# Optimization experiments

Hardware: AMD Instinct MI355X
Metric: run time of the kernel (lower is better)

Reference implementation:

```python
import jax, jax.numpy as jnp
import numpy as np

B, S, M_DIM, N_DIM, K_NNZ = 8, 2048, 2048, 2048, 205


def setup_inputs() -> dict:
    key = jax.random.key(0)
    k1, k2, k3, k4 = jax.random.split(key, 4)
    x = jax.random.normal(k1, (B, S, M_DIM), dtype=jnp.float32)
    # CSR structure: K_NNZ unique, sorted column indices per row
    scores = jax.random.uniform(k2, (N_DIM, M_DIM))
    cols = jnp.sort(jnp.argsort(scores, axis=1)[:, :K_NNZ], axis=1)  # [N, K] unique per row
    indices = cols.reshape(-1).astype(jnp.int32)                      # [nnz]
    indptr = (jnp.arange(N_DIM + 1) * K_NNZ).astype(jnp.int32)        # [N+1]
    W_val = jax.random.normal(k3, (N_DIM * K_NNZ,), dtype=jnp.float32) * (1.0 / np.sqrt(M_DIM))
    bias = jax.random.normal(k4, (N_DIM,), dtype=jnp.float32) * 0.01
    return {"x": x, "W_val": W_val, "bias": bias, "indices": indices, "indptr": indptr}


def reference(x, W_val, bias, indices, indptr):
    # SparseLinear.forward: y = x @ W^T + bias, with W stored in CSR
    # (W_val: nnz values, indptr: [N+1] row pointers, indices: [nnz] column ids).
    N = indptr.shape[0] - 1
    M = x.shape[-1]
    nnz = W_val.shape[0]
    # row id of each nonzero, derived from indptr (standard CSR expansion)
    row_ids = jnp.searchsorted(indptr, jnp.arange(nnz, dtype=indptr.dtype), side="right") - 1
    # materialize the sparse weight (CSR columns are unique per row -> set is exact)
    W = jnp.zeros((N, M), dtype=W_val.dtype).at[row_ids, indices].set(W_val)
    return jnp.einsum("bsm,nm->bsn", x, W) + bias
```

## Files before the change

### kernel.cpp

```cpp
#include <hip/hip_runtime.h>
#include <hip/hip_bf16.h>
#include <stdint.h>

#define M_TOT 16384
#define K_TOT 2048
#define N_TOT 2048

#define BM 128
#define BN 128
#define BK 64

#define W_BLOCKS 2048
#define CAST_BLOCKS 16384

typedef __attribute__((ext_vector_type(8))) short short8;
typedef __attribute__((ext_vector_type(4))) float float4v;
typedef __attribute__((ext_vector_type(8))) unsigned short ushort8;

__device__ __forceinline__ unsigned short f2bf_rne(float f) {
    union { float f; unsigned u; } a; a.f = f;
    unsigned r = a.u + 0x7FFFu + ((a.u >> 16) & 1u);
    return (unsigned short)(r >> 16);
}

__global__ void prep_kernel(const float* __restrict__ x,
                            const float* __restrict__ val, const int* __restrict__ idx,
                            const int* __restrict__ indptr,
                            unsigned short* __restrict__ xb, unsigned short* __restrict__ Wb) {
    const int b = blockIdx.x;
    if (b < W_BLOCKS) {
        const int n = b;
        unsigned short* row = Wb + (size_t)n * K_TOT;
        ushort8 z = {0, 0, 0, 0, 0, 0, 0, 0};
        ((ushort8*)row)[threadIdx.x] = z;
        __syncthreads();
        const int s = indptr[n], e = indptr[n + 1];
        for (int j = s + (int)threadIdx.x; j < e; j += (int)blockDim.x)
            row[idx[j]] = f2bf_rne(val[j]);
    } else {
        const int i = (b - W_BLOCKS) * 256 + (int)threadIdx.x;
        const float4* xf = (const float4*)x;
        float4 a = xf[2 * i];
        float4 c = xf[2 * i + 1];
        ushort8 o;
        o[0] = f2bf_rne(a.x); o[1] = f2bf_rne(a.y); o[2] = f2bf_rne(a.z); o[3] = f2bf_rne(a.w);
        o[4] = f2bf_rne(c.x); o[5] = f2bf_rne(c.y); o[6] = f2bf_rne(c.z); o[7] = f2bf_rne(c.w);
        ((ushort8*)xb)[i] = o;
    }
}

__global__ __launch_bounds__(256) void gemm_bias_kernel(
    const unsigned short* __restrict__ A,
    const unsigned short* __restrict__ Bw,
    const float* __restrict__ bias,
    float* __restrict__ C)
{
    __shared__ unsigned short Asm[BM * BK];
    __shared__ unsigned short Bsm[BN * BK];

    const int tid  = threadIdx.x;
    const int lane = tid & 63;
    const int wave = tid >> 6;
    const int bm = blockIdx.y;
    const int bn = blockIdx.x;

    const int srow_l = lane >> 3;
    const int schunk = ((lane & 7) ^ srow_l) * 8;
    const unsigned short* a_g[4];
    const unsigned short* b_g[4];
    unsigned short* a_l[4];
    unsigned short* b_l[4];
#pragma unroll
    for (int l = 0; l < 4; ++l) {
        const int row = wave * 32 + l * 8 + srow_l;
        a_g[l] = A  + (size_t)(bm * BM + row) * K_TOT + schunk;
        b_g[l] = Bw + (size_t)(bn * BN + row) * K_TOT + schunk;
        a_l[l] = Asm + (wave * 32 + l * 8) * BK;
        b_l[l] = Bsm + (wave * 32 + l * 8) * BK;
    }

    const int wm = (wave >> 1) * 64;
    const int wn = (wave & 1) * 64;
    const int mrow = lane & 15;
    const int quad = lane >> 4;
    const int rx   = mrow & 7;

    float4v acc[4][4] = {};

    for (int k0 = 0; k0 < K_TOT; k0 += BK) {
        __syncthreads();
#pragma unroll
        for (int l = 0; l < 4; ++l)
            __builtin_amdgcn_global_load_lds(
                (const __attribute__((address_space(1))) unsigned int*)(a_g[l] + k0),
                (__attribute__((address_space(3))) unsigned int*)a_l[l], 16, 0, 0);
#pragma unroll
        for (int l = 0; l < 4; ++l)
            __builtin_amdgcn_global_load_lds(
                (const __attribute__((address_space(1))) unsigned int*)(b_g[l] + k0),
                (__attribute__((address_space(3))) unsigned int*)b_l[l], 16, 0, 0);
        __syncthreads();

#pragma unroll
        for (int ks = 0; ks < 2; ++ks) {
            short8 af[4], bf_[4];
#pragma unroll
            for (int mi = 0; mi < 4; ++mi) {
                const int r = wm + mi * 16 + mrow;
                const int slot = (ks * 4 + quad) ^ rx;
                af[mi] = *(const short8*)(Asm + r * BK + slot * 8);
            }
#pragma unroll
            for (int ni = 0; ni < 4; ++ni) {
                const int r = wn + ni * 16 + mrow;
                const int slot = (ks * 4 + quad) ^ rx;
                bf_[ni] = *(const short8*)(Bsm + r * BK + slot * 8);
            }
#pragma unroll
            for (int mi = 0; mi < 4; ++mi)
#pragma unroll
                for (int ni = 0; ni < 4; ++ni)
                    acc[mi][ni] = __builtin_amdgcn_mfma_f32_16x16x32_bf16(
                        af[mi], bf_[ni], acc[mi][ni], 0, 0, 0);
        }
    }

#pragma unroll
    for (int ni = 0; ni < 4; ++ni) {
        const int col = bn * BN + wn + ni * 16 + mrow;
        const float bv = bias[col];
#pragma unroll
        for (int mi = 0; mi < 4; ++mi) {
#pragma unroll
            for (int r = 0; r < 4; ++r) {
                const int row = bm * BM + wm + mi * 16 + quad * 4 + r;
                C[(size_t)row * N_TOT + col] = acc[mi][ni][r] + bv;
            }
        }
    }
}

extern "C" void kernel_launch(void* const* d_in, const int* in_sizes, int n_in,
                              void* d_out, int out_size, void* d_ws, size_t ws_size,
                              hipStream_t stream) {
    const float* x       = (const float*)d_in[0];
    const float* W_val   = (const float*)d_in[1];
    const float* bias    = (const float*)d_in[2];
    const int*   indices = (const int*)d_in[3];
    const int*   indptr  = (const int*)d_in[4];
    float* out = (float*)d_out;

    unsigned short* xb = (unsigned short*)d_ws;
    unsigned short* Wb = xb + (size_t)M_TOT * K_TOT;
    if (ws_size < ((size_t)M_TOT * K_TOT + (size_t)N_TOT * K_TOT) * sizeof(unsigned short))
        return;

    prep_kernel<<<W_BLOCKS + CAST_BLOCKS, 256, 0, stream>>>(x, W_val, indices, indptr, xb, Wb);
    dim3 grid(N_TOT / BN, M_TOT / BM);
    gemm_bias_kernel<<<grid, 256, 0, stream>>>(xb, Wb, bias, out);
}
```

Measured before the change: 372.8 us.

## Add 256x256 double-buffered 8-wave GEMM with phased prefetch and tile swizzle

Adds a new GEMM kernel with 256x256 tiles, 512 threads and 128KB of dynamic LDS. It double-buffers A and B halves and interleaves global-to-LDS prefetch with MFMA phases, using barriers and explicit vmcnt waits. Block indices are remapped for L2 locality, and setprio is raised during MFMA. The aim is to hide load latency and raise arithmetic intensity, at the cost of occupancy and complex hand synchronisation. The old 128x128 kernel is kept as a fallback if the shared-memory attribute call fails.

```diff
diff --git a/kernel.cpp b/kernel.cpp
--- a/kernel.cpp
+++ b/kernel.cpp
@@ -6,9 +6,10 @@
 #define K_TOT 2048
 #define N_TOT 2048
 
-#define BM 128
-#define BN 128
+#define BM 256
+#define BN 256
 #define BK 64
+#define LDS_HALF (128 * 64)
 
 #define W_BLOCKS 2048
 #define CAST_BLOCKS 16384
@@ -49,14 +50,163 @@
     }
 }
 
-__global__ __launch_bounds__(256) void gemm_bias_kernel(
+__global__ __launch_bounds__(512, 2) void gemm_bias_kernel_256(
     const unsigned short* __restrict__ A,
     const unsigned short* __restrict__ Bw,
     const float* __restrict__ bias,
     float* __restrict__ C)
 {
-    __shared__ unsigned short Asm[BM * BK];
-    __shared__ unsigned short Bsm[BN * BK];
+    extern __shared__ unsigned short lds[];
+
+    const int tid  = threadIdx.x;
+    const int lane = tid & 63;
+    const int wave = tid >> 6;
+
+    const int raw = blockIdx.x;
+    const int lid = (raw & 7) * 64 + (raw >> 3);
+    const int bm = lid >> 3;
+    const int bn = lid & 7;
+
+    const int wrow = wave >> 2;
+    const int wcol = wave & 3;
+    const int wr16 = wrow * 16;
+    const int wc16 = wcol * 16;
+    const int mrow = lane & 15;
+    const int quad = lane >> 4;
+    const int rx   = mrow & 7;
+
+    const int srow = lane >> 3;
+    const int csrc = ((lane & 7) ^ srow) * 8;
+    const unsigned short* pA = A  + (size_t)(bm * BM + wave * 8 + srow) * K_TOT + csrc;
+    const unsigned short* pB = Bw + (size_t)(bn * BN + wave * 8 + srow) * K_TOT + csrc;
+    unsigned short* lw = lds + wave * 8 * 64;
+
+    float4v acc[8][4] = {};
+
+#define STAGE(PG, MATIDX, BUF, H, K0)                                            \
+    { _Pragma("unroll")                                                          \
+      for (int l = 0; l < 2; ++l) {                                              \
+        const unsigned short* g = (PG) + ((size_t)((H) * 128 + l * 64) * K_TOT + (size_t)(K0)); \
+        unsigned short* lp = lw + (((BUF) * 4 + (MATIDX) * 2 + (H)) * LDS_HALF) + l * 64 * 64;  \
+        __builtin_amdgcn_global_load_lds(                                        \
+            (const __attribute__((address_space(1))) unsigned int*)g,            \
+            (__attribute__((address_space(3))) unsigned int*)lp, 16, 0, 0);      \
+      } }
+
+#define WAITV4 asm volatile("s_waitcnt vmcnt(4)" ::: "memory")
+#define WAITV0 asm volatile("s_waitcnt vmcnt(0)" ::: "memory")
+#define NOSTG  ((void)0)
+#define NOWT   ((void)0)
+
+#define PHASE(BUF, MH, NH, STG, TAILW)                                           \
+  {                                                                              \
+    const unsigned short* Ah = lds + ((BUF) * 4 + (MH)) * LDS_HALF;              \
+    const unsigned short* Bh = lds + ((BUF) * 4 + 2 + (NH)) * LDS_HALF;          \
+    short8 af[4][2], bfr[2][2];                                                  \
+    _Pragma("unroll")                                                            \
+    for (int mi = 0; mi < 4; ++mi) {                                             \
+      const int r = mi * 32 + wr16 + mrow;                                       \
+      _Pragma("unroll")                                                          \
+      for (int ks = 0; ks < 2; ++ks)                                             \
+        af[mi][ks] = *(const short8*)(Ah + r * 64 + (((ks * 4 + quad) ^ rx) * 8)); \
+    }                                                                            \
+    _Pragma("unroll")                                                            \
+    for (int ni = 0; ni < 2; ++ni) {                                             \
+      const int r = ni * 64 + wc16 + mrow;                                       \
+      _Pragma("unroll")                                                          \
+      for (int ks = 0; ks < 2; ++ks)                                             \
+        bfr[ni][ks] = *(const short8*)(Bh + r * 64 + (((ks * 4 + quad) ^ rx) * 8)); \
+    }                                                                            \
+    STG;                                                                         \
+    asm volatile("" ::: "memory");                                               \
+    __builtin_amdgcn_s_barrier();                                                \
+    asm volatile("s_waitcnt lgkmcnt(0)" ::: "memory");                           \
+    __builtin_amdgcn_s_setprio(1);                                               \
+    _Pragma("unroll")                                                            \
+    for (int mi = 0; mi < 4; ++mi)                                               \
+      _Pragma("unroll")                                                          \
+      for (int ni = 0; ni < 2; ++ni)                                             \
+        _Pragma("unroll")                                                        \
+        for (int ks = 0; ks < 2; ++ks)                                           \
+          acc[(MH) * 4 + mi][(NH) * 2 + ni] =                                    \
+              __builtin_amdgcn_mfma_f32_16x16x32_bf16(                           \
+                  af[mi][ks], bfr[ni][ks], acc[(MH) * 4 + mi][(NH) * 2 + ni], 0, 0, 0); \
+    __builtin_amdgcn_s_setprio(0);                                               \
+    TAILW;                                                                       \
+    asm volatile("" ::: "memory");                                               \
+    __builtin_amdgcn_s_barrier();                                                \
+    asm volatile("" ::: "memory");                                               \
+  }
+
+    STAGE(pA, 0, 0, 0, 0);
+    STAGE(pB, 1, 0, 1, 0);
+    STAGE(pB, 1, 0, 0, 0);
+    STAGE(pA, 0, 0, 1, 0);
+    STAGE(pA, 0, 1, 0, 64);
+    STAGE(pB, 1, 1, 1, 64);
+    WAITV4;
+    asm volatile("" ::: "memory");
+    __builtin_amdgcn_s_barrier();
+    asm volatile("" ::: "memory");
+
+    int k0b = 64, k0c = 128, k0d = 192;
+#pragma unroll 1
+    for (int it = 0; it < 15; ++it) {
+        PHASE(0, 0, 0, STAGE(pB, 1, 1, 0, k0b), NOWT)
+        PHASE(0, 0, 1, STAGE(pA, 0, 1, 1, k0b), NOWT)
+        PHASE(0, 1, 1, STAGE(pA, 0, 0, 0, k0c), NOWT)
+        PHASE(0, 1, 0, STAGE(pB, 1, 0, 1, k0c), WAITV4)
+        PHASE(1, 0, 0, STAGE(pB, 1, 0, 0, k0c), NOWT)
+        PHASE(1, 0, 1, STAGE(pA, 0, 0, 1, k0c), NOWT)
+        PHASE(1, 1, 1, STAGE(pA, 0, 1, 0, k0d), NOWT)
+        PHASE(1, 1, 0, STAGE(pB, 1, 1, 1, k0d), WAITV4)
+        k0b += 128; k0c += 128; k0d += 128;
+    }
+    PHASE(0, 0, 0, STAGE(pB, 1, 1, 0, k0b), NOWT)
+    PHASE(0, 0, 1, STAGE(pA, 0, 1, 1, k0b), NOWT)
+    PHASE(0, 1, 1, NOSTG, NOWT)
+    PHASE(0, 1, 0, NOSTG, WAITV0)
+    PHASE(1, 0, 0, NOSTG, NOWT)
+    PHASE(1, 0, 1, NOSTG, NOWT)
+    PHASE(1, 1, 1, NOSTG, NOWT)
+    PHASE(1, 1, 0, NOSTG, NOWT)
+
+#pragma unroll
+    for (int nh = 0; nh < 2; ++nh)
+#pragma unroll
+        for (int ni = 0; ni < 2; ++ni) {
+            const int col = bn * BN + nh * 128 + ni * 64 + wc16 + mrow;
+            const float bv = bias[col];
+#pragma unroll
+            for (int mh = 0; mh < 2; ++mh)
+#pragma unroll
+                for (int mi = 0; mi < 4; ++mi) {
+                    const int row0 = bm * BM + mh * 128 + mi * 32 + wr16 + quad * 4;
+#pragma unroll
+                    for (int r = 0; r < 4; ++r)
+                        C[(size_t)(row0 + r) * N_TOT + col] =
+                            acc[mh * 4 + mi][nh * 2 + ni][r] + bv;
+                }
+        }
+#undef PHASE
+#undef STAGE
+#undef WAITV4
+#undef WAITV0
+#undef NOSTG
+#undef NOWT
+}
+
+#define FBM 128
+#define FBN 128
+#define FBK 64
+__global__ __launch_bounds__(256) void gemm_bias_kernel_128(
+    const unsigned short* __restrict__ A,
+    const unsigned short* __restrict__ Bw,
+    const float* __restrict__ bias,
+    float* __restrict__ C)
+{
+    __shared__ unsigned short Asm[FBM * FBK];
+    __shared__ unsigned short Bsm[FBN * FBK];
 
     const int tid  = threadIdx.x;
     const int lane = tid & 63;
@@ -73,10 +223,10 @@
 #pragma unroll
     for (int l = 0; l < 4; ++l) {
         const int row = wave * 32 + l * 8 + srow_l;
-        a_g[l] = A  + (size_t)(bm * BM + row) * K_TOT + schunk;
-        b_g[l] = Bw + (size_t)(bn * BN + row) * K_TOT + schunk;
-        a_l[l] = Asm + (wave * 32 + l * 8) * BK;
-        b_l[l] = Bsm + (wave * 32 + l * 8) * BK;
+        a_g[l] = A  + (size_t)(bm * FBM + row) * K_TOT + schunk;
+        b_g[l] = Bw + (size_t)(bn * FBN + row) * K_TOT + schunk;
+        a_l[l] = Asm + (wave * 32 + l * 8) * FBK;
+        b_l[l] = Bsm + (wave * 32 + l * 8) * FBK;
     }
 
     const int wm = (wave >> 1) * 64;
@@ -87,7 +237,7 @@
 
     float4v acc[4][4] = {};
 
-    for (int k0 = 0; k0 < K_TOT; k0 += BK) {
+    for (int k0 = 0; k0 < K_TOT; k0 += FBK) {
         __syncthreads();
 #pragma unroll
         for (int l = 0; l < 4; ++l)
@@ -108,13 +258,13 @@
             for (int mi = 0; mi < 4; ++mi) {
                 const int r = wm + mi * 16 + mrow;
                 const int slot = (ks * 4 + quad) ^ rx;
-                af[mi] = *(const short8*)(Asm + r * BK + slot * 8);
+                af[mi] = *(const short8*)(Asm + r * FBK + slot * 8);
             }
 #pragma unroll
             for (int ni = 0; ni < 4; ++ni) {
                 const int r = wn + ni * 16 + mrow;
                 const int slot = (ks * 4 + quad) ^ rx;
-                bf_[ni] = *(const short8*)(Bsm + r * BK + slot * 8);
+                bf_[ni] = *(const short8*)(Bsm + r * FBK + slot * 8);
             }
 #pragma unroll
             for (int mi = 0; mi < 4; ++mi)
@@ -127,13 +277,13 @@
 
 #pragma unroll
     for (int ni = 0; ni < 4; ++ni) {
-        const int col = bn * BN + wn + ni * 16 + mrow;
+        const int col = bn * FBN + wn + ni * 16 + mrow;
         const float bv = bias[col];
 #pragma unroll
         for (int mi = 0; mi < 4; ++mi) {
 #pragma unroll
             for (int r = 0; r < 4; ++r) {
-                const int row = bm * BM + wm + mi * 16 + quad * 4 + r;
+                const int row = bm * FBM + wm + mi * 16 + quad * 4 + r;
                 C[(size_t)row * N_TOT + col] = acc[mi][ni][r] + bv;
             }
         }
@@ -155,7 +305,16 @@
     if (ws_size < ((size_t)M_TOT * K_TOT + (size_t)N_TOT * K_TOT) * sizeof(unsigned short))
         return;
 
+    hipError_t attr_ok = hipFuncSetAttribute(
+        reinterpret_cast<const void*>(gemm_bias_kernel_256),
+        hipFuncAttributeMaxDynamicSharedMemorySize, 131072);
+
     prep_kernel<<<W_BLOCKS + CAST_BLOCKS, 256, 0, stream>>>(x, W_val, indices, indptr, xb, Wb);
-    dim3 grid(N_TOT / BN, M_TOT / BM);
-    gemm_bias_kernel<<<grid, 256, 0, stream>>>(xb, Wb, bias, out);
-}
+
+    if (attr_ok == hipSuccess) {
+        gemm_bias_kernel_256<<<dim3(512), 512, 131072, stream>>>(xb, Wb, bias, out);
+    } else {
+        dim3 grid(N_TOT / FBN, M_TOT / FBM);
+        gemm_bias_kernel_128<<<grid, 256, 0, stream>>>(xb, Wb, bias, out);
+    }
+}
```

After: 355.6 us. 1.05x faster.
